# Kernel tuning notes

Hardware: AMD Instinct MI355X
Metric: run time of the kernel (lower is better)

The kernel has to match this reference:

```python
import jax, jax.numpy as jnp
import numpy as np

EPS = 1e-6

def _ln(x, g, b):
    m = jnp.mean(x, -1, keepdims=True)
    v = jnp.mean((x - m) ** 2, -1, keepdims=True)
    return (x - m) * jax.lax.rsqrt(v + 1e-5) * g + b

def _mha(qin, kin, vin, wq, bq, wk, bk, wv, bv, wo, bo, nh=8):
    B, T, D = qin.shape
    S = kin.shape[1]
    dh = D // nh
    q = (qin @ wq + bq).reshape(B, T, nh, dh)
    k = (kin @ wk + bk).reshape(B, S, nh, dh)
    v = (vin @ wv + bv).reshape(B, S, nh, dh)
    a = jax.nn.softmax(jnp.einsum('bthd,bshd->bhts', q, k) / np.float32(np.sqrt(dh)), -1)
    o = jnp.einsum('bhts,bshd->bthd', a, v).reshape(B, T, D)
    return o @ wo + bo

def _sinu_pe(pos, num_feats=128, temperature=20.0):
    # pos: [..., 2] (x, y); returns [..., 2*num_feats] ordered (y-feats, x-feats)
    dim_t = temperature ** ((2 * (jnp.arange(num_feats) // 2)) / num_feats)
    e = pos[..., None] * (2 * np.pi) / dim_t  # [..., 2, F]
    e = jnp.stack([jnp.sin(e[..., 0::2]), jnp.cos(e[..., 1::2])], -1).reshape(e.shape)
    return jnp.concatenate([e[..., 1, :], e[..., 0, :]], -1)

def _spatial36(b1, b2, sizes):
    # b1, b2: [B, Q, 4]; sizes: [B, 2] = (h, w). UPT-style 18 feats + log -> 36.
    h = sizes[:, 0:1]; w = sizes[:, 1:2]
    c1x = (b1[..., 0] + b1[..., 2]) / 2; c1y = (b1[..., 1] + b1[..., 3]) / 2
    c2x = (b2[..., 0] + b2[..., 2]) / 2; c2y = (b2[..., 1] + b2[..., 3]) / 2
    w1 = b1[..., 2] - b1[..., 0]; h1 = b1[..., 3] - b1[..., 1]
    w2 = b2[..., 2] - b2[..., 0]; h2 = b2[..., 3] - b2[..., 1]
    a1 = w1 * h1; a2 = w2 * h2
    dx = jnp.abs(c2x - c1x) / (w1 + EPS)
    dy = jnp.abs(c2y - c1y) / (h1 + EPS)
    ix = jnp.clip(jnp.minimum(b1[..., 2], b2[..., 2]) - jnp.maximum(b1[..., 0], b2[..., 0]), 0)
    iy = jnp.clip(jnp.minimum(b1[..., 3], b2[..., 3]) - jnp.maximum(b1[..., 1], b2[..., 1]), 0)
    inter = ix * iy
    iou = inter / (a1 + a2 - inter + EPS)
    f = jnp.stack([c1x / w, c1y / h, c2x / w, c2y / h, w1 / w, h1 / h, w2 / w, h2 / h,
                   a1 / (h * w), a2 / (h * w), a2 / (a1 + EPS), w1 / (h1 + EPS), w2 / (h2 + EPS), iou,
                   (c2x > c1x) * dx, (c2x < c1x) * dx, (c2y > c1y) * dy, (c2y < c1y) * dy], -1)
    return jnp.concatenate([f, jnp.log(f + EPS)], -1)

def _forward(boxes, embeds, image_sizes, pose, line, sw1, sb1, sw2, sb2, sw3, sb3, bw, bb, pw, pb, lw, lb, enc_pe_w, enc_pe_b, enc_qkv_w, enc_qkv_b, enc_out_w, enc_out_b, enc_ff1_w, enc_ff1_b, enc_ff2_w, enc_ff2_b, enc_ln1_g, enc_ln1_b, enc_ln2_g, enc_ln2_b, dec_q_w, dec_q_b, dec_kv_w, dec_kv_b, dec_out_w, dec_out_b, dec_ff1_w, dec_ff1_b, dec_ff2_w, dec_ff2_b, dec_ln1_g, dec_ln1_b, dec_ln2_g, dec_ln2_b, fc1_w, fc1_b, fc2_w, fc2_b, mln1_g, mln1_b, mln2_g, mln2_b, m1_w, m1_b, m2_w, m2_b, labels, nh):
    B, N, _ = boxes.shape
    # static human-object pairing (x != y) & (x < nh)
    xg, yg = np.meshgrid(np.arange(N), np.arange(N), indexing='ij')
    keep = (xg != yg) & (xg < nh)
    xk = jnp.asarray(xg[keep]); yk = jnp.asarray(yg[keep])  # [P]
    # line features: adaptive-avg-pool(1,1) + 1x1 conv == spatial mean + linear
    line_feat = jnp.mean(line, axis=(2, 3)) @ lw + lb  # [B, 256]
    # spatial head on all N*N ordered pairs, then gather kept pairs
    xa = jnp.asarray(xg.reshape(-1)); ya = jnp.asarray(yg.reshape(-1))
    f36 = _spatial36(boxes[:, xa], boxes[:, ya], image_sizes)  # [B, N*N, 36]
    s = jax.nn.relu(f36 @ sw1 + sb1)
    s = jax.nn.relu(s @ sw2 + sb2)
    s = jax.nn.relu(s @ sw3 + sb3)
    spa = s.reshape(B, N, N, -1)[:, xk, yk]  # [B, P, R]
    # box sinusoidal positional encodings (cat of centre-PE and wh-PE)
    whwh = image_sizes[:, jnp.array([1, 0, 1, 0])][:, None]  # [B,1,4]
    bxn = boxes / whwh
    ctr = (bxn[..., :2] + bxn[..., 2:]) / 2
    whb = bxn[..., 2:] - bxn[..., :2]
    box_pe = jnp.concatenate([_sinu_pe(ctr), _sinu_pe(whb)], -1)  # [B, N, 512]
    # 2-layer transformer encoder over instance tokens (pos added to q,k)
    posx = box_pe @ enc_pe_w + enc_pe_b
    x = embeds
    for i in range(enc_qkv_w.shape[0]):
        wq, wk_, wv = jnp.split(enc_qkv_w[i], 3, axis=1)
        bq, bk_, bv = jnp.split(enc_qkv_b[i], 3)
        qk = x + posx
        att = _mha(qk, qk, x, wq, bq, wk_, bk_, wv, bv, enc_out_w[i], enc_out_b[i])
        x = _ln(x + att, enc_ln1_g[i], enc_ln1_b[i])
        ff = jax.nn.relu(x @ enc_ff1_w[i] + enc_ff1_b[i]) @ enc_ff2_w[i] + enc_ff2_b[i]
        x = _ln(x + ff, enc_ln2_g[i], enc_ln2_b[i])
    # pair gather + human/object positional embeds (box PE projected + line feature)
    pe_h = box_pe[:, xk] @ bw + bb + line_feat[:, None, :]
    pe_o = box_pe[:, yk] @ bw + bb + line_feat[:, None, :]
    h = x[:, xk]; o = x[:, yk]  # [B, P, 256]
    pose_ctx = pose @ pw + pb  # [B, M, 256]
    # HO refine decoder: cross-attention from pair tokens to pose tokens
    for l in range(dec_q_w.shape[0]):
        wk_, wv = jnp.split(dec_kv_w[l], 2, axis=1)
        bk_, bv = jnp.split(dec_kv_b[l], 2)
        def _layer(feat, pe):
            att = _mha(feat + pe, pose_ctx, pose_ctx, dec_q_w[l], dec_q_b[l], wk_, bk_, wv, bv, dec_out_w[l], dec_out_b[l])
            feat = _ln(feat + att, dec_ln1_g[l], dec_ln1_b[l])
            ff = jax.nn.relu(feat @ dec_ff1_w[l] + dec_ff1_b[l]) @ dec_ff2_w[l] + dec_ff2_b[l]
            return _ln(feat + ff, dec_ln2_g[l], dec_ln2_b[l])
        h = _layer(h, pe_h)
        o = _layer(o, pe_o)
    # multi-modal fusion
    ho = jnp.concatenate([h, o], -1)  # [B, P, 512]
    ho = _ln(ho @ fc1_w + fc1_b, mln1_g, mln1_b)
    sp = _ln(spa @ fc2_w + fc2_b, mln2_g, mln2_b)
    z = jax.nn.relu(jnp.concatenate([ho, sp], -1))
    z = jax.nn.relu(z @ m1_w + m1_b)
    z = jax.nn.relu(z @ m2_w + m2_b)
    return z  # [B, P, 256] HOI query features

def setup_inputs() -> dict:
    key = jax.random.key(0)
    ks = iter(jax.random.split(key, 80))
    B, N, NH, M, HH, WW = 16, 128, 32, 64, 8, 8
    W = 0.05
    def rn(shape, s=1.0):
        return jax.random.normal(next(ks), shape, dtype=jnp.float32) * s
    def ru(shape):
        return jax.random.uniform(next(ks), shape, dtype=jnp.float32)
    sizes = 800.0 + 480.0 * ru((B, 2))  # (h, w)
    wh = sizes[:, jnp.array([1, 0])]
    xy = ru((B, N, 2)) * wh[:, None] * 0.7
    bwh = ru((B, N, 2)) * wh[:, None] * 0.25 + 4.0
    boxes = jnp.concatenate([xy, xy + bwh], -1)
    labels = jnp.concatenate([jnp.zeros((B, NH), jnp.int32), jax.random.randint(next(ks), (B, N - NH), 1, 81, dtype=jnp.int32)], -1)
    return dict(
        boxes=boxes, embeds=rn((B, N, 256)), image_sizes=sizes, pose=rn((B, M, 768)), line=rn((B, 2048, HH, WW)),
        sw1=rn((36, 128), W), sb1=jnp.zeros((128,)), sw2=rn((128, 256), W), sb2=jnp.zeros((256,)), sw3=rn((256, 256), W), sb3=jnp.zeros((256,)),
        bw=rn((512, 256), W), bb=jnp.zeros((256,)), pw=rn((768, 256), W), pb=jnp.zeros((256,)), lw=rn((2048, 256), W), lb=jnp.zeros((256,)),
        enc_pe_w=rn((512, 256), W), enc_pe_b=jnp.zeros((256,)),
        enc_qkv_w=rn((2, 256, 768), W), enc_qkv_b=jnp.zeros((2, 768)), enc_out_w=rn((2, 256, 256), W), enc_out_b=jnp.zeros((2, 256)),
        enc_ff1_w=rn((2, 256, 1024), W), enc_ff1_b=jnp.zeros((2, 1024)), enc_ff2_w=rn((2, 1024, 256), W), enc_ff2_b=jnp.zeros((2, 256)),
        enc_ln1_g=jnp.ones((2, 256)), enc_ln1_b=jnp.zeros((2, 256)), enc_ln2_g=jnp.ones((2, 256)), enc_ln2_b=jnp.zeros((2, 256)),
        dec_q_w=rn((2, 256, 256), W), dec_q_b=jnp.zeros((2, 256)), dec_kv_w=rn((2, 256, 512), W), dec_kv_b=jnp.zeros((2, 512)),
        dec_out_w=rn((2, 256, 256), W), dec_out_b=jnp.zeros((2, 256)),
        dec_ff1_w=rn((2, 256, 1024), W), dec_ff1_b=jnp.zeros((2, 1024)), dec_ff2_w=rn((2, 1024, 256), W), dec_ff2_b=jnp.zeros((2, 256)),
        dec_ln1_g=jnp.ones((2, 256)), dec_ln1_b=jnp.zeros((2, 256)), dec_ln2_g=jnp.ones((2, 256)), dec_ln2_b=jnp.zeros((2, 256)),
        fc1_w=rn((512, 256), W), fc1_b=jnp.zeros((256,)), fc2_w=rn((256, 256), W), fc2_b=jnp.zeros((256,)),
        mln1_g=jnp.ones((256,)), mln1_b=jnp.zeros((256,)), mln2_g=jnp.ones((256,)), mln2_b=jnp.zeros((256,)),
        m1_w=rn((512, 384), W), m1_b=jnp.zeros((384,)), m2_w=rn((384, 256), W), m2_b=jnp.zeros((256,)),
        labels=labels, nh=NH)

def reference(boxes, embeds, image_sizes, pose, line, sw1, sb1, sw2, sb2, sw3, sb3, bw, bb, pw, pb, lw, lb, enc_pe_w, enc_pe_b, enc_qkv_w, enc_qkv_b, enc_out_w, enc_out_b, enc_ff1_w, enc_ff1_b, enc_ff2_w, enc_ff2_b, enc_ln1_g, enc_ln1_b, enc_ln2_g, enc_ln2_b, dec_q_w, dec_q_b, dec_kv_w, dec_kv_b, dec_out_w, dec_out_b, dec_ff1_w, dec_ff1_b, dec_ff2_w, dec_ff2_b, dec_ln1_g, dec_ln1_b, dec_ln2_g, dec_ln2_b, fc1_w, fc1_b, fc2_w, fc2_b, mln1_g, mln1_b, mln2_g, mln2_b, m1_w, m1_b, m2_w, m2_b, labels, nh):
    return _forward(boxes, embeds, image_sizes, pose, line, sw1, sb1, sw2, sb2, sw3, sb3, bw, bb, pw, pb, lw, lb, enc_pe_w, enc_pe_b, enc_qkv_w, enc_qkv_b, enc_out_w, enc_out_b, enc_ff1_w, enc_ff1_b, enc_ff2_w, enc_ff2_b, enc_ln1_g, enc_ln1_b, enc_ln2_g, enc_ln2_b, dec_q_w, dec_q_b, dec_kv_w, dec_kv_b, dec_out_w, dec_out_b, dec_ff1_w, dec_ff1_b, dec_ff2_w, dec_ff2_b, dec_ln1_g, dec_ln1_b, dec_ln2_g, dec_ln2_b, fc1_w, fc1_b, fc2_w, fc2_b, mln1_g, mln1_b, mln2_g, mln2_b, m1_w, m1_b, m2_w, m2_b, labels, nh)
```

## Files before the change

kernel.cpp:

```cpp
#include <hip/hip_runtime.h>
#include <stdint.h>

static constexpr int B      = 16;
static constexpr int N      = 128;
static constexpr int P      = 4064;
static constexpr int MPOSE  = 64;
static constexpr int64_t BN = (int64_t)B * N;
static constexpr int64_t BP = (int64_t)B * P;

#define TWO_PI 6.283185307179586f
#define QSCALE 0.17677669529663687f

typedef __attribute__((ext_vector_type(4))) float f32x4;
typedef __attribute__((ext_vector_type(8))) short bf16x8;
typedef __attribute__((ext_vector_type(8))) unsigned short u16x8;
typedef __attribute__((ext_vector_type(4))) unsigned short u16x4;

__device__ __forceinline__ unsigned short f2bf(float f) {
    union { float f; unsigned u; } v; v.f = f;
    unsigned r = (v.u + 0x7fffu + ((v.u >> 16) & 1u)) >> 16;
    return (unsigned short)r;
}
__device__ __forceinline__ float bf2f(unsigned short u) {
    union { unsigned u; float f; } v; v.u = (unsigned)u << 16;
    return v.f;
}
__device__ __forceinline__ void pair_xy(int p, int& x, int& y) {
    x = p / 127;
    int r = p - x * 127;
    y = (r < x) ? r : r + 1;
}

struct WDesc { const float* src; int64_t dstOff; int K, Nn, Kpad, blockStart; };
struct WTable { WDesc d[29]; int nDesc; };

__global__ __launch_bounds__(256) void wprep_all_k(WTable t, unsigned short* __restrict__ wt)
{
    __shared__ float s[32][33];
    int bid = blockIdx.x;
    int di = 0;
    for (int i = 1; i < t.nDesc; ++i) if (t.d[i].blockStart <= bid) di = i;
    const WDesc& d = t.d[di];
    int lbid = bid - d.blockStart;
    int kTiles = d.Kpad >> 5;
    int k0 = (lbid % kTiles) * 32, n0 = (lbid / kTiles) * 32;
    int tx = threadIdx.x & 31, ty = threadIdx.x >> 5;
#pragma unroll
    for (int i = 0; i < 4; ++i) {
        int k = k0 + ty + i * 8;
        s[ty + i * 8][tx] = (k < d.K) ? d.src[(int64_t)k * d.Nn + n0 + tx] : 0.f;
    }
    __syncthreads();
    unsigned short* dst = wt + d.dstOff;
#pragma unroll
    for (int i = 0; i < 4; ++i) {
        int n = n0 + ty + i * 8;
        dst[(int64_t)n * d.Kpad + k0 + tx] = f2bf(s[tx][ty + i * 8]);
    }
}

template <bool RELU_OUT>
__global__ __launch_bounds__(256) void bgemm_k(
    const float* __restrict__ A, const float* __restrict__ A2, int lda,
    const unsigned short* __restrict__ Bt, int ldk,
    const float* __restrict__ bias,
    const float* __restrict__ Cadd, int addLd,
    const float* __restrict__ lfp,
    float* __restrict__ C, int ldc,
    int kSteps)
{
    __shared__ unsigned short As[128][40];
    __shared__ unsigned short Bs[128][40];
    const int tid  = threadIdx.x;
    const int lane = tid & 63;
    const int wave = tid >> 6;
    const int wr = wave >> 1, wc = wave & 1;
    const int row0 = blockIdx.y * 128, col0 = blockIdx.x * 128;
    const int l15 = lane & 15, l4 = lane >> 4;
    const int sr = tid >> 1;
    const int sh = (tid & 1) * 16;

    f32x4 acc[4][4] = {};

    for (int ks = 0; ks < kSteps; ++ks) {
        const int k0 = ks * 32;
        {
            const int64_t off = (int64_t)(row0 + sr) * lda + k0 + sh;
            const float* ap = A + off;
            float v[16];
#pragma unroll
            for (int i = 0; i < 4; ++i) {
                float4 tv = ((const float4*)ap)[i];
                v[i*4+0] = tv.x; v[i*4+1] = tv.y; v[i*4+2] = tv.z; v[i*4+3] = tv.w;
            }
            if (A2) {
                const float* ap2 = A2 + off;
#pragma unroll
                for (int i = 0; i < 4; ++i) {
                    float4 tv = ((const float4*)ap2)[i];
                    v[i*4+0] += tv.x; v[i*4+1] += tv.y; v[i*4+2] += tv.z; v[i*4+3] += tv.w;
                }
            }
            u16x8 p0, p1;
#pragma unroll
            for (int j = 0; j < 8; ++j) { p0[j] = f2bf(v[j]); p1[j] = f2bf(v[8 + j]); }
            *(u16x8*)&As[sr][sh]     = p0;
            *(u16x8*)&As[sr][sh + 8] = p1;
        }
        {
            const unsigned short* bp = Bt + (int64_t)(col0 + sr) * ldk + k0 + sh;
            *(u16x8*)&Bs[sr][sh]     = *(const u16x8*)bp;
            *(u16x8*)&Bs[sr][sh + 8] = *(const u16x8*)(bp + 8);
        }
        __syncthreads();
        bf16x8 af[4], bfr[4];
#pragma unroll
        for (int f = 0; f < 4; ++f) {
            af[f]  = *(const bf16x8*)&As[wr * 64 + f * 16 + l15][l4 * 8];
            bfr[f] = *(const bf16x8*)&Bs[wc * 64 + f * 16 + l15][l4 * 8];
        }
#pragma unroll
        for (int i = 0; i < 4; ++i)
#pragma unroll
            for (int j = 0; j < 4; ++j)
                acc[i][j] = __builtin_amdgcn_mfma_f32_16x16x32_bf16(af[i], bfr[j], acc[i][j], 0, 0, 0);
        __syncthreads();
    }
#pragma unroll
    for (int i = 0; i < 4; ++i) {
        int rb = row0 + wr * 64 + i * 16 + l4 * 4;
#pragma unroll
        for (int j = 0; j < 4; ++j) {
            int c = col0 + wc * 64 + j * 16 + l15;
            float bv = bias ? bias[c] : 0.f;
#pragma unroll
            for (int e = 0; e < 4; ++e) {
                int r = rb + e;
                float vv = acc[i][j][e] + bv;
                if (Cadd && c < addLd) vv += Cadd[(int64_t)r * addLd + c];
                if (lfp) vv += lfp[(r >> 7) * 256 + c];
                if (RELU_OUT) vv = fmaxf(vv, 0.f);
                C[(int64_t)r * ldc + c] = vv;
            }
        }
    }
}

static void bgemm(hipStream_t st,
                  const float* A, const float* A2, int lda,
                  const unsigned short* Bt, int ldk, const float* bias,
                  const float* Cadd, int addLd, const float* lfp,
                  float* C, int ldc, int M, int Ncols, int K, bool reluOut)
{
    dim3 g(Ncols / 128, M / 128), b(256);
    if (reluOut) bgemm_k<true><<<g,b,0,st>>>(A,A2,lda,Bt,ldk,bias,Cadd,addLd,lfp,C,ldc,K/32);
    else         bgemm_k<false><<<g,b,0,st>>>(A,A2,lda,Bt,ldk,bias,Cadd,addLd,lfp,C,ldc,K/32);
}

__global__ __launch_bounds__(256) void tgemm_k(
    const float* __restrict__ A, int lda,
    const unsigned short* __restrict__ Bt, int ldk,
    const float* __restrict__ bias,
    const float* __restrict__ res,
    const float* __restrict__ g, const float* __restrict__ be,
    float* __restrict__ C, int kSteps)
{
    __shared__ unsigned short As[64][40];
    __shared__ unsigned short Bs[256][40];
    __shared__ float partS[64][4], partQ[64][4];
    __shared__ float statM[64], statI[64];
    const int tid = threadIdx.x;
    const int lane = tid & 63, w = tid >> 6;
    const int l15 = lane & 15, l4 = lane >> 4;
    const int row0 = blockIdx.x * 64;
    const int sra = tid >> 2, sha = (tid & 3) * 8;

    f32x4 acc[4][4] = {};
    for (int ks = 0; ks < kSteps; ++ks) {
        int k0 = ks * 32;
        {
            const float* ap = A + (int64_t)(row0 + sra) * lda + k0 + sha;
            float4 t0 = ((const float4*)ap)[0];
            float4 t1 = ((const float4*)ap)[1];
            u16x8 p;
            p[0]=f2bf(t0.x); p[1]=f2bf(t0.y); p[2]=f2bf(t0.z); p[3]=f2bf(t0.w);
            p[4]=f2bf(t1.x); p[5]=f2bf(t1.y); p[6]=f2bf(t1.z); p[7]=f2bf(t1.w);
            *(u16x8*)&As[sra][sha] = p;
        }
        {
            const unsigned short* bp = Bt + (int64_t)tid * ldk + k0;
#pragma unroll
            for (int q = 0; q < 4; ++q)
                *(u16x8*)&Bs[tid][q * 8] = *(const u16x8*)(bp + q * 8);
        }
        __syncthreads();
        bf16x8 af[4], bfr[4];
#pragma unroll
        for (int f = 0; f < 4; ++f) {
            af[f]  = *(const bf16x8*)&As[f * 16 + l15][l4 * 8];
            bfr[f] = *(const bf16x8*)&Bs[w * 64 + f * 16 + l15][l4 * 8];
        }
#pragma unroll
        for (int i = 0; i < 4; ++i)
#pragma unroll
            for (int j = 0; j < 4; ++j)
                acc[i][j] = __builtin_amdgcn_mfma_f32_16x16x32_bf16(af[i], bfr[j], acc[i][j], 0, 0, 0);
        __syncthreads();
    }
    float ps[4][4] = {}, pq[4][4] = {};
#pragma unroll
    for (int i = 0; i < 4; ++i)
#pragma unroll
    for (int j = 0; j < 4; ++j) {
        int c = w * 64 + j * 16 + l15;
#pragma unroll
        for (int e = 0; e < 4; ++e) {
            int r = i * 16 + l4 * 4 + e;
            float v = acc[i][j][e] + bias[c] + res[(int64_t)(row0 + r) * 256 + c];
            acc[i][j][e] = v;
            ps[i][e] += v;
            pq[i][e] += v * v;
        }
    }
#pragma unroll
    for (int i = 0; i < 4; ++i)
#pragma unroll
    for (int e = 0; e < 4; ++e) {
#pragma unroll
        for (int m = 1; m < 16; m <<= 1) {
            ps[i][e] += __shfl_xor(ps[i][e], m);
            pq[i][e] += __shfl_xor(pq[i][e], m);
        }
    }
    if (l15 == 0) {
#pragma unroll
        for (int i = 0; i < 4; ++i)
#pragma unroll
        for (int e = 0; e < 4; ++e) {
            int r = i * 16 + l4 * 4 + e;
            partS[r][w] = ps[i][e];
            partQ[r][w] = pq[i][e];
        }
    }
    __syncthreads();
    if (tid < 64) {
        float s = partS[tid][0] + partS[tid][1] + partS[tid][2] + partS[tid][3];
        float q = partQ[tid][0] + partQ[tid][1] + partQ[tid][2] + partQ[tid][3];
        float m = s * (1.f/256.f);
        float var = q * (1.f/256.f) - m * m;
        statM[tid] = m;
        statI[tid] = rsqrtf(var + 1e-5f);
    }
    __syncthreads();
#pragma unroll
    for (int i = 0; i < 4; ++i)
#pragma unroll
    for (int j = 0; j < 4; ++j) {
        int c = w * 64 + j * 16 + l15;
#pragma unroll
        for (int e = 0; e < 4; ++e) {
            int r = i * 16 + l4 * 4 + e;
            C[(int64_t)(row0 + r) * 256 + c] = (acc[i][j][e] - statM[r]) * statI[r] * g[c] + be[c];
        }
    }
}

template <bool RELU_OUT, bool RELU_A, bool OUT_BF16>
__global__ __launch_bounds__(256) void hgemm_k(
    const unsigned short* __restrict__ A, int lda,
    const unsigned short* __restrict__ Bt, int ldk,
    const float* __restrict__ bias,
    void* __restrict__ Cv, int ldc,
    int kSteps)
{
    __shared__ unsigned short As[128][40];
    __shared__ unsigned short Bs[128][40];
    const int tid  = threadIdx.x;
    const int lane = tid & 63;
    const int wave = tid >> 6;
    const int wr = wave >> 1, wc = wave & 1;
    const int row0 = blockIdx.y * 128, col0 = blockIdx.x * 128;
    const int l15 = lane & 15, l4 = lane >> 4;
    const int sr = tid >> 1;
    const int sh = (tid & 1) * 16;

    f32x4 acc[4][4] = {};

    for (int ks = 0; ks < kSteps; ++ks) {
        const int k0 = ks * 32;
        {
            const unsigned short* ap = A + (int64_t)(row0 + sr) * lda + k0 + sh;
            u16x8 q0 = *(const u16x8*)ap;
            u16x8 q1 = *(const u16x8*)(ap + 8);
            if (RELU_A) {
#pragma unroll
                for (int q = 0; q < 8; ++q) {
                    q0[q] = (q0[q] & 0x8000u) ? 0 : q0[q];
                    q1[q] = (q1[q] & 0x8000u) ? 0 : q1[q];
                }
            }
            *(u16x8*)&As[sr][sh]     = q0;
            *(u16x8*)&As[sr][sh + 8] = q1;
        }
        {
            const unsigned short* bp = Bt + (int64_t)(col0 + sr) * ldk + k0 + sh;
            *(u16x8*)&Bs[sr][sh]     = *(const u16x8*)bp;
            *(u16x8*)&Bs[sr][sh + 8] = *(const u16x8*)(bp + 8);
        }
        __syncthreads();
        bf16x8 af[4], bfr[4];
#pragma unroll
        for (int f = 0; f < 4; ++f) {
            af[f]  = *(const bf16x8*)&As[wr * 64 + f * 16 + l15][l4 * 8];
            bfr[f] = *(const bf16x8*)&Bs[wc * 64 + f * 16 + l15][l4 * 8];
        }
#pragma unroll
        for (int i = 0; i < 4; ++i)
#pragma unroll
            for (int j = 0; j < 4; ++j)
                acc[i][j] = __builtin_amdgcn_mfma_f32_16x16x32_bf16(af[i], bfr[j], acc[i][j], 0, 0, 0);
        __syncthreads();
    }
#pragma unroll
    for (int i = 0; i < 4; ++i) {
        int rb = row0 + wr * 64 + i * 16 + l4 * 4;
#pragma unroll
        for (int j = 0; j < 4; ++j) {
            int c = col0 + wc * 64 + j * 16 + l15;
            float bv = bias ? bias[c] : 0.f;
#pragma unroll
            for (int e = 0; e < 4; ++e) {
                int64_t off = (int64_t)(rb + e) * ldc + c;
                float vv = acc[i][j][e] + bv;
                if (RELU_OUT) vv = fmaxf(vv, 0.f);
                if (OUT_BF16) ((unsigned short*)Cv)[off] = f2bf(vv);
                else          ((float*)Cv)[off] = vv;
            }
        }
    }
}

__global__ __launch_bounds__(256) void spa_k(
    const float* __restrict__ boxes, const float* __restrict__ sizes,
    const unsigned short* __restrict__ W1, const float* __restrict__ b1,
    const unsigned short* __restrict__ W2, const float* __restrict__ b2,
    unsigned short* __restrict__ t3out, int chunk0)
{
    __shared__ unsigned short F[128][72];
    __shared__ unsigned short Bs[128][40];
    __shared__ unsigned short D1s[128][136];
    const int tid  = threadIdx.x;
    const int lane = tid & 63;
    const int wave = tid >> 6;
    const int wr = wave >> 1, wc = wave & 1;
    const int row0 = blockIdx.x * 128;
    const int l15 = lane & 15, l4 = lane >> 4;
    const int sr = tid >> 1;
    const int sh = (tid & 1) * 16;

    if (tid < 128) {
        int gp = chunk0 + row0 + tid;
        int b = gp / P, p = gp - b * P;
        int xi, yi; pair_xy(p, xi, yi);
        const float* b1x = boxes + ((int64_t)b * N + xi) * 4;
        const float* b2x = boxes + ((int64_t)b * N + yi) * 4;
        float h = sizes[b * 2 + 0], w = sizes[b * 2 + 1];
        float c1x = (b1x[0] + b1x[2]) * 0.5f, c1y = (b1x[1] + b1x[3]) * 0.5f;
        float c2x = (b2x[0] + b2x[2]) * 0.5f, c2y = (b2x[1] + b2x[3]) * 0.5f;
        float w1 = b1x[2] - b1x[0], h1 = b1x[3] - b1x[1];
        float w2 = b2x[2] - b2x[0], h2 = b2x[3] - b2x[1];
        float a1 = w1 * h1, a2 = w2 * h2;
        float dx = fabsf(c2x - c1x) / (w1 + 1e-6f);
        float dy = fabsf(c2y - c1y) / (h1 + 1e-6f);
        float ix = fmaxf(fminf(b1x[2], b2x[2]) - fmaxf(b1x[0], b2x[0]), 0.f);
        float iy = fmaxf(fminf(b1x[3], b2x[3]) - fmaxf(b1x[1], b2x[1]), 0.f);
        float inter = ix * iy;
        float iou = inter / (a1 + a2 - inter + 1e-6f);
        float f[18];
        f[0] = c1x / w;  f[1] = c1y / h;  f[2] = c2x / w;  f[3] = c2y / h;
        f[4] = w1 / w;   f[5] = h1 / h;   f[6] = w2 / w;   f[7] = h2 / h;
        f[8] = a1 / (h * w); f[9] = a2 / (h * w); f[10] = a2 / (a1 + 1e-6f);
        f[11] = w1 / (h1 + 1e-6f); f[12] = w2 / (h2 + 1e-6f); f[13] = iou;
        f[14] = (c2x > c1x) ? dx : 0.f;  f[15] = (c2x < c1x) ? dx : 0.f;
        f[16] = (c2y > c1y) ? dy : 0.f;  f[17] = (c2y < c1y) ? dy : 0.f;
#pragma unroll
        for (int i = 0; i < 18; ++i) {
            F[tid][i]      = f2bf(f[i]);
            F[tid][18 + i] = f2bf(logf(f[i] + 1e-6f));
        }
#pragma unroll
        for (int i = 36; i < 64; ++i) F[tid][i] = 0;
    }
    __syncthreads();

    f32x4 acc1[4][4] = {};
    for (int ks = 0; ks < 2; ++ks) {
        const int k0 = ks * 32;
        {
            const unsigned short* bp = W1 + (int64_t)sr * 64 + k0 + sh;
            *(u16x8*)&Bs[sr][sh]     = *(const u16x8*)bp;
            *(u16x8*)&Bs[sr][sh + 8] = *(const u16x8*)(bp + 8);
        }
        __syncthreads();
        bf16x8 af[4], bfr[4];
#pragma unroll
        for (int f = 0; f < 4; ++f) {
            af[f]  = *(const bf16x8*)&F[wr * 64 + f * 16 + l15][k0 + l4 * 8];
            bfr[f] = *(const bf16x8*)&Bs[wc * 64 + f * 16 + l15][l4 * 8];
        }
#pragma unroll
        for (int i = 0; i < 4; ++i)
#pragma unroll
            for (int j = 0; j < 4; ++j)
                acc1[i][j] = __builtin_amdgcn_mfma_f32_16x16x32_bf16(af[i], bfr[j], acc1[i][j], 0, 0, 0);
        __syncthreads();
    }
#pragma unroll
    for (int i = 0; i < 4; ++i) {
        int rb = wr * 64 + i * 16 + l4 * 4;
#pragma unroll
        for (int j = 0; j < 4; ++j) {
            int c = wc * 64 + j * 16 + l15;
            float bv = b1[c];
#pragma unroll
            for (int e = 0; e < 4; ++e)
                D1s[rb + e][c] = f2bf(fmaxf(acc1[i][j][e] + bv, 0.f));
        }
    }
    __syncthreads();

    f32x4 acc2[2][4][4] = {};
#pragma unroll
    for (int n = 0; n < 2; ++n) {
        for (int kk = 0; kk < 4; ++kk) {
            {
                const unsigned short* bp = W2 + (int64_t)(n * 128 + sr) * 128 + kk * 32 + sh;
                *(u16x8*)&Bs[sr][sh]     = *(const u16x8*)bp;
                *(u16x8*)&Bs[sr][sh + 8] = *(const u16x8*)(bp + 8);
            }
            __syncthreads();
            bf16x8 af[4], bfr[4];
#pragma unroll
            for (int f = 0; f < 4; ++f) {
                af[f]  = *(const bf16x8*)&D1s[wr * 64 + f * 16 + l15][kk * 32 + l4 * 8];
                bfr[f] = *(const bf16x8*)&Bs[wc * 64 + f * 16 + l15][l4 * 8];
            }
#pragma unroll
            for (int i = 0; i < 4; ++i)
#pragma unroll
                for (int j = 0; j < 4; ++j)
                    acc2[n][i][j] = __builtin_amdgcn_mfma_f32_16x16x32_bf16(af[i], bfr[j], acc2[n][i][j], 0, 0, 0);
            __syncthreads();
        }
    }
#pragma unroll
    for (int n = 0; n < 2; ++n)
#pragma unroll
    for (int i = 0; i < 4; ++i) {
        int rb = row0 + wr * 64 + i * 16 + l4 * 4;
#pragma unroll
        for (int j = 0; j < 4; ++j) {
            int c = n * 128 + wc * 64 + j * 16 + l15;
            float bv = b2[c];
#pragma unroll
            for (int e = 0; e < 4; ++e)
                t3out[(int64_t)(rb + e) * 256 + c] = f2bf(fmaxf(acc2[n][i][j][e] + bv, 0.f));
        }
    }
}

__global__ __launch_bounds__(256) void sw3fc2ln_k(
    const unsigned short* __restrict__ A,
    const unsigned short* __restrict__ W1, const float* __restrict__ b1,
    const unsigned short* __restrict__ W2, const float* __restrict__ b2,
    const float* __restrict__ g, const float* __restrict__ be,
    unsigned short* __restrict__ outp, int ldo)
{
    __shared__ unsigned short As[128][40];
    __shared__ unsigned short Bs[128][40];
    __shared__ unsigned short D1s[128][136];
    __shared__ float partS[128][2], partQ[128][2];
    __shared__ float statM[128], statI[128];
    const int tid  = threadIdx.x;
    const int lane = tid & 63;
    const int wave = tid >> 6;
    const int wr = wave >> 1, wc = wave & 1;
    const int row0 = blockIdx.x * 128;
    const int l15 = lane & 15, l4 = lane >> 4;
    const int sr = tid >> 1;
    const int sh = (tid & 1) * 16;

    f32x4 acc2[2][4][4] = {};
    for (int j = 0; j < 2; ++j) {
        f32x4 acc1[4][4] = {};
        for (int ks = 0; ks < 8; ++ks) {
            const int k0 = ks * 32;
            {
                const unsigned short* ap = A + (int64_t)(row0 + sr) * 256 + k0 + sh;
                *(u16x8*)&As[sr][sh]     = *(const u16x8*)ap;
                *(u16x8*)&As[sr][sh + 8] = *(const u16x8*)(ap + 8);
            }
            {
                const unsigned short* bp = W1 + (int64_t)(j * 128 + sr) * 256 + k0 + sh;
                *(u16x8*)&Bs[sr][sh]     = *(const u16x8*)bp;
                *(u16x8*)&Bs[sr][sh + 8] = *(const u16x8*)(bp + 8);
            }
            __syncthreads();
            bf16x8 af[4], bfr[4];
#pragma unroll
            for (int f = 0; f < 4; ++f) {
                af[f]  = *(const bf16x8*)&As[wr * 64 + f * 16 + l15][l4 * 8];
                bfr[f] = *(const bf16x8*)&Bs[wc * 64 + f * 16 + l15][l4 * 8];
            }
#pragma unroll
            for (int i = 0; i < 4; ++i)
#pragma unroll
                for (int jj = 0; jj < 4; ++jj)
                    acc1[i][jj] = __builtin_amdgcn_mfma_f32_16x16x32_bf16(af[i], bfr[jj], acc1[i][jj], 0, 0, 0);
            __syncthreads();
        }
#pragma unroll
        for (int i = 0; i < 4; ++i) {
            int rb = wr * 64 + i * 16 + l4 * 4;
#pragma unroll
            for (int jj = 0; jj < 4; ++jj) {
                int c = wc * 64 + jj * 16 + l15;
                float bv = b1[j * 128 + c];
#pragma unroll
                for (int e = 0; e < 4; ++e)
                    D1s[rb + e][c] = f2bf(fmaxf(acc1[i][jj][e] + bv, 0.f));
            }
        }
        __syncthreads();
#pragma unroll
        for (int n = 0; n < 2; ++n) {
            for (int kk = 0; kk < 4; ++kk) {
                {
                    const unsigned short* bp = W2 + (int64_t)(n * 128 + sr) * 256 + j * 128 + kk * 32 + sh;
                    *(u16x8*)&Bs[sr][sh]     = *(const u16x8*)bp;
                    *(u16x8*)&Bs[sr][sh + 8] = *(const u16x8*)(bp + 8);
                }
                __syncthreads();
                bf16x8 af[4], bfr[4];
#pragma unroll
                for (int f = 0; f < 4; ++f) {
                    af[f]  = *(const bf16x8*)&D1s[wr * 64 + f * 16 + l15][kk * 32 + l4 * 8];
                    bfr[f] = *(const bf16x8*)&Bs[wc * 64 + f * 16 + l15][l4 * 8];
                }
#pragma unroll
                for (int i = 0; i < 4; ++i)
#pragma unroll
                    for (int jj = 0; jj < 4; ++jj)
                        acc2[n][i][jj] = __builtin_amdgcn_mfma_f32_16x16x32_bf16(af[i], bfr[jj], acc2[n][i][jj], 0, 0, 0);
                __syncthreads();
            }
        }
    }
    float ps[4][4] = {}, pq[4][4] = {};
#pragma unroll
    for (int n = 0; n < 2; ++n)
#pragma unroll
    for (int i = 0; i < 4; ++i)
#pragma unroll
    for (int jj = 0; jj < 4; ++jj) {
        int c = n * 128 + wc * 64 + jj * 16 + l15;
#pragma unroll
        for (int e = 0; e < 4; ++e) {
            float v = acc2[n][i][jj][e] + b2[c];
            acc2[n][i][jj][e] = v;
            ps[i][e] += v;
            pq[i][e] += v * v;
        }
    }
#pragma unroll
    for (int i = 0; i < 4; ++i)
#pragma unroll
    for (int e = 0; e < 4; ++e) {
#pragma unroll
        for (int m = 1; m < 16; m <<= 1) {
            ps[i][e] += __shfl_xor(ps[i][e], m);
            pq[i][e] += __shfl_xor(pq[i][e], m);
        }
    }
    if (l15 == 0) {
#pragma unroll
        for (int i = 0; i < 4; ++i)
#pragma unroll
        for (int e = 0; e < 4; ++e) {
            int r = wr * 64 + i * 16 + l4 * 4 + e;
            partS[r][wc] = ps[i][e];
            partQ[r][wc] = pq[i][e];
        }
    }
    __syncthreads();
    if (tid < 128) {
        float s = partS[tid][0] + partS[tid][1];
        float q = partQ[tid][0] + partQ[tid][1];
        float m = s * (1.f/256.f);
        float var = q * (1.f/256.f) - m * m;
        statM[tid] = m;
        statI[tid] = rsqrtf(var + 1e-5f);
    }
    __syncthreads();
#pragma unroll
    for (int n = 0; n < 2; ++n)
#pragma unroll
    for (int i = 0; i < 4; ++i)
#pragma unroll
    for (int jj = 0; jj < 4; ++jj) {
        int c = n * 128 + wc * 64 + jj * 16 + l15;
#pragma unroll
        for (int e = 0; e < 4; ++e) {
            int r = wr * 64 + i * 16 + l4 * 4 + e;
            float o = (acc2[n][i][jj][e] - statM[r]) * statI[r] * g[c] + be[c];
            outp[(int64_t)(row0 + r) * ldo + c] = f2bf(o);
        }
    }
}

__global__ __launch_bounds__(256) void pairln_k(
    const float* __restrict__ UV, const float* __restrict__ fb,
    const float* __restrict__ g, const float* __restrict__ be,
    unsigned short* __restrict__ outp, int ldo, int chunk0, int rows)
{
    int wave = threadIdx.x >> 6, lane = threadIdx.x & 63;
    int li = blockIdx.x * 4 + wave;
    if (li >= rows) return;
    int gp = chunk0 + li;
    int b = gp / P, p = gp - b * P;
    int xi, yi; pair_xy(p, xi, yi);
    int c = lane * 4;
    float4 u  = *(const float4*)(UV + ((int64_t)(b * 128 + xi)) * 512 + c);
    float4 vv = *(const float4*)(UV + ((int64_t)(b * 128 + yi)) * 512 + 256 + c);
    float4 fbv = *(const float4*)(fb + c);
    float4 v;
    v.x = u.x + vv.x + fbv.x; v.y = u.y + vv.y + fbv.y;
    v.z = u.z + vv.z + fbv.z; v.w = u.w + vv.w + fbv.w;
    float s  = v.x + v.y + v.z + v.w;
    float sq = v.x*v.x + v.y*v.y + v.z*v.z + v.w*v.w;
#pragma unroll
    for (int off = 1; off < 64; off <<= 1) {
        s  += __shfl_xor(s, off);
        sq += __shfl_xor(sq, off);
    }
    float m = s * (1.f/256.f);
    float var = sq * (1.f/256.f) - m * m;
    float inv = rsqrtf(var + 1e-5f);
    float4 gg = *(const float4*)(g + c);
    float4 bb = *(const float4*)(be + c);
    u16x4 o;
    o[0] = f2bf((v.x - m) * inv * gg.x + bb.x);
    o[1] = f2bf((v.y - m) * inv * gg.y + bb.y);
    o[2] = f2bf((v.z - m) * inv * gg.z + bb.z);
    o[3] = f2bf((v.w - m) * inv * gg.w + bb.w);
    *(u16x4*)(outp + (int64_t)li * ldo + c) = o;
}

__global__ __launch_bounds__(256) void line_mean_k(const float* __restrict__ line, float* __restrict__ lm)
{
    int wave = threadIdx.x >> 6, lane = threadIdx.x & 63;
    int bc = blockIdx.x * 4 + wave;
    float v = line[(int64_t)bc * 64 + lane];
#pragma unroll
    for (int off = 1; off < 64; off <<= 1) v += __shfl_xor(v, off);
    if (lane == 0) lm[bc] = v * (1.f/64.f);
}

__global__ __launch_bounds__(256) void line_proj_k(
    const float* __restrict__ lm, const float* __restrict__ lw,
    const float* __restrict__ lb, float* __restrict__ lf)
{
    __shared__ float red[8][32];
    int b = blockIdx.y, jg = blockIdx.x;
    int jj = threadIdx.x & 31, cc = threadIdx.x >> 5;
    int j = jg * 32 + jj;
    const float* lmb = lm + (int64_t)b * 2048 + cc * 256;
    const float* lwp = lw + (int64_t)(cc * 256) * 256 + j;
    float acc = 0.f;
#pragma unroll 4
    for (int k = 0; k < 256; ++k) acc += lmb[k] * lwp[(int64_t)k * 256];
    red[cc][jj] = acc;
    __syncthreads();
    if (cc == 0) {
        float s = lb[j];
#pragma unroll
        for (int i = 0; i < 8; ++i) s += red[i][jj];
        lf[b * 256 + j] = s;
    }
}

__global__ __launch_bounds__(512) void boxpe_k(
    const float* __restrict__ boxes, const float* __restrict__ sizes, float* __restrict__ boxpe)
{
    int row = blockIdx.x;
    int b = row >> 7;
    int i = threadIdx.x;
    const float* bx = boxes + (int64_t)row * 4;
    float h = sizes[b * 2 + 0], w = sizes[b * 2 + 1];
    float x0 = bx[0] / w, y0 = bx[1] / h, x1 = bx[2] / w, y1 = bx[3] / h;
    int seg = i >> 7, j = i & 127, k = j >> 1;
    float val;
    switch (seg) {
        case 0: val = (y0 + y1) * 0.5f; break;
        case 1: val = (x0 + x1) * 0.5f; break;
        case 2: val = (y1 - y0); break;
        default: val = (x1 - x0); break;
    }
    float dimt = exp2f((float)k * (4.321928094887362f / 64.f));
    float arg = val * TWO_PI / dimt;
    boxpe[(int64_t)row * 512 + i] = (j & 1) ? cosf(arg) : sinf(arg);
}

__global__ __launch_bounds__(128) void enc_attn_k(
    const float* __restrict__ qkv, float* __restrict__ outp)
{
    int b = blockIdx.x >> 3, hd = blockIdx.x & 7;
    __shared__ float kl[128][32];
    __shared__ float vl[128][32];
    int tid = threadIdx.x;
    for (int i = tid; i < 128 * 32; i += 128) {
        int s = i >> 5, j = i & 31;
        const float* rp = qkv + ((int64_t)(b * 128 + s)) * 768 + hd * 32 + j;
        kl[s][j] = rp[256];
        vl[s][j] = rp[512];
    }
    __syncthreads();
    int t = tid;
    const float* qp = qkv + ((int64_t)(b * 128 + t)) * 768 + hd * 32;
    float qr[32];
#pragma unroll
    for (int j = 0; j < 32; ++j) qr[j] = qp[j] * QSCALE;
    float m = -1e30f, l = 0.f;
    for (int s = 0; s < 128; ++s) {
        float d = 0.f;
#pragma unroll
        for (int j = 0; j < 32; ++j) d += qr[j] * kl[s][j];
        float mn = fmaxf(m, d);
        l = l * __expf(m - mn) + __expf(d - mn);
        m = mn;
    }
    float acc[32] = {};
    for (int s = 0; s < 128; ++s) {
        float d = 0.f;
#pragma unroll
        for (int j = 0; j < 32; ++j) d += qr[j] * kl[s][j];
        float wgt = __expf(d - m);
#pragma unroll
        for (int j = 0; j < 32; ++j) acc[j] += wgt * vl[s][j];
    }
    float linv = 1.f / l;
    float* op = outp + ((int64_t)(b * 128 + t)) * 256 + hd * 32;
#pragma unroll
    for (int j = 0; j < 32; ++j) op[j] = acc[j] * linv;
}

__global__ __launch_bounds__(256) void dec_attn_k(
    const float* __restrict__ q, const float* __restrict__ kv,
    float* __restrict__ outp, int rows, int rpb)
{
    int hd = blockIdx.y;
    int r0 = blockIdx.x * 256;
    __shared__ float kl[2][64][32];
    __shared__ float vl[2][64][32];
    int tid = threadIdx.x;
    int b0 = r0 / rpb;
    int b1 = (r0 + 255) / rpb;
    if (b1 >= B) b1 = B - 1;
    for (int i = tid; i < 64 * 32; i += 256) {
        int s = i >> 5, j = i & 31;
        int64_t off0 = ((int64_t)(b0 * MPOSE + s)) * 512 + hd * 32 + j;
        int64_t off1 = ((int64_t)(b1 * MPOSE + s)) * 512 + hd * 32 + j;
        kl[0][s][j] = kv[off0];
        vl[0][s][j] = kv[off0 + 256];
        kl[1][s][j] = kv[off1];
        vl[1][s][j] = kv[off1 + 256];
    }
    __syncthreads();
    int r = r0 + tid;
    if (r >= rows) return;
    int which = (r / rpb == b0) ? 0 : 1;
    int64_t qoff = (int64_t)r * 256 + hd * 32;
    float qr[32];
#pragma unroll
    for (int j = 0; j < 32; ++j) qr[j] = q[qoff + j] * QSCALE;
    float m = -1e30f, l = 0.f;
    for (int s = 0; s < 64; ++s) {
        float d = 0.f;
#pragma unroll
        for (int j = 0; j < 32; ++j) d += qr[j] * kl[which][s][j];
        float mn = fmaxf(m, d);
        l = l * __expf(m - mn) + __expf(d - mn);
        m = mn;
    }
    float acc[32] = {};
    for (int s = 0; s < 64; ++s) {
        float d = 0.f;
#pragma unroll
        for (int j = 0; j < 32; ++j) d += qr[j] * kl[which][s][j];
        float wgt = __expf(d - m);
#pragma unroll
        for (int j = 0; j < 32; ++j) acc[j] += wgt * vl[which][s][j];
    }
    float linv = 1.f / l;
#pragma unroll
    for (int j = 0; j < 32; ++j) outp[qoff + j] = acc[j] * linv;
}

static constexpr int64_t WT_QKV  = 0;
static constexpr int64_t WT_EOUT = WT_QKV  + 2*196608;
static constexpr int64_t WT_EFF1 = WT_EOUT + 2*65536;
static constexpr int64_t WT_EFF2 = WT_EFF1 + 2*262144;
static constexpr int64_t WT_DQ   = WT_EFF2 + 2*262144;
static constexpr int64_t WT_DKV  = WT_DQ   + 2*65536;
static constexpr int64_t WT_DOUT = WT_DKV  + 2*131072;
static constexpr int64_t WT_DFF1 = WT_DOUT + 2*65536;
static constexpr int64_t WT_DFF2 = WT_DFF1 + 2*262144;
static constexpr int64_t WT_SW1  = WT_DFF2 + 2*262144;
static constexpr int64_t WT_SW2  = WT_SW1 + 8192;
static constexpr int64_t WT_SW3  = WT_SW2 + 32768;
static constexpr int64_t WT_BW   = WT_SW3 + 65536;
static constexpr int64_t WT_PW   = WT_BW  + 131072;
static constexpr int64_t WT_EPE  = WT_PW  + 196608;
static constexpr int64_t WT_FC1  = WT_EPE + 131072;
static constexpr int64_t WT_FC2  = WT_FC1 + 131072;
static constexpr int64_t WT_M1   = WT_FC2 + 65536;
static constexpr int64_t WT_M2   = WT_M1  + 196608;
static constexpr int64_t WT_TOTAL = WT_M2 + 98304;

extern "C" void kernel_launch(void* const* d_in, const int* in_sizes, int n_in,
                              void* d_out, int out_size, void* d_ws, size_t ws_size,
                              hipStream_t stream)
{
    (void)in_sizes; (void)n_in; (void)out_size;
    const float* boxes     = (const float*)d_in[0];
    const float* embeds    = (const float*)d_in[1];
    const float* sizes     = (const float*)d_in[2];
    const float* pose      = (const float*)d_in[3];
    const float* line      = (const float*)d_in[4];
    const float* sw1 = (const float*)d_in[5];  const float* sb1 = (const float*)d_in[6];
    const float* sw2 = (const float*)d_in[7];  const float* sb2 = (const float*)d_in[8];
    const float* sw3 = (const float*)d_in[9];  const float* sb3 = (const float*)d_in[10];
    const float* bw  = (const float*)d_in[11]; const float* bb  = (const float*)d_in[12];
    const float* pw  = (const float*)d_in[13]; const float* pb  = (const float*)d_in[14];
    const float* lw  = (const float*)d_in[15]; const float* lb  = (const float*)d_in[16];
    const float* enc_pe_w  = (const float*)d_in[17]; const float* enc_pe_b = (const float*)d_in[18];
    const float* enc_qkv_w = (const float*)d_in[19]; const float* enc_qkv_b = (const float*)d_in[20];
    const float* enc_out_w = (const float*)d_in[21]; const float* enc_out_b = (const float*)d_in[22];
    const float* enc_ff1_w = (const float*)d_in[23]; const float* enc_ff1_b = (const float*)d_in[24];
    const float* enc_ff2_w = (const float*)d_in[25]; const float* enc_ff2_b = (const float*)d_in[26];
    const float* enc_ln1_g = (const float*)d_in[27]; const float* enc_ln1_b = (const float*)d_in[28];
    const float* enc_ln2_g = (const float*)d_in[29]; const float* enc_ln2_b = (const float*)d_in[30];
    const float* dec_q_w   = (const float*)d_in[31]; const float* dec_q_b  = (const float*)d_in[32];
    const float* dec_kv_w  = (const float*)d_in[33]; const float* dec_kv_b = (const float*)d_in[34];
    const float* dec_out_w = (const float*)d_in[35]; const float* dec_out_b = (const float*)d_in[36];
    const float* dec_ff1_w = (const float*)d_in[37]; const float* dec_ff1_b = (const float*)d_in[38];
    const float* dec_ff2_w = (const float*)d_in[39]; const float* dec_ff2_b = (const float*)d_in[40];
    const float* dec_ln1_g = (const float*)d_in[41]; const float* dec_ln1_b = (const float*)d_in[42];
    const float* dec_ln2_g = (const float*)d_in[43]; const float* dec_ln2_b = (const float*)d_in[44];
    const float* fc1_w = (const float*)d_in[45]; const float* fc1_b = (const float*)d_in[46];
    const float* fc2_w = (const float*)d_in[47]; const float* fc2_b = (const float*)d_in[48];
    const float* mln1_g = (const float*)d_in[49]; const float* mln1_b = (const float*)d_in[50];
    const float* mln2_g = (const float*)d_in[51]; const float* mln2_b = (const float*)d_in[52];
    const float* m1_w = (const float*)d_in[53]; const float* m1_b = (const float*)d_in[54];
    const float* m2_w = (const float*)d_in[55]; const float* m2_b = (const float*)d_in[56];
    float* out = (float*)d_out;

    float* base = (float*)d_ws;
    int64_t wsf = (int64_t)(ws_size / sizeof(float));
    float* x_   = base;
    float* bpw_ = x_   + 524288;
    float* lf   = bpw_ + 524288;
    float* kv0  = lf   + 4096;
    unsigned short* wt = (unsigned short*)(kv0 + 2 * 524288);
    float* arena = (float*)(wt + WT_TOTAL);
    const int64_t LIVE_F = arena - base;
    int64_t arena_f = wsf - LIVE_F;
    if (arena_f < 0) arena_f = 0;

    float* posx  = arena;
    float* boxpe = posx  + 524288;
    float* pqk0  = boxpe + 1048576;
    float* pqk1  = pqk0  + 1048576;
    float* e_qkv = pqk1  + 1048576;
    float* e_t   = e_qkv + 1572864;
    float* e_ff  = e_t   + 524288;
    float* pctx  = e_ff  + 2097152;
    float* lm    = pctx  + 262144;

    int64_t rc = ((arena_f * 2) / 1152) & ~127LL;
    if (rc > BP) rc = BP;
    if (rc < 128) rc = 128;

    {
        WTable T;
        int nd = 0, bs = 0;
        auto add = [&](const float* src, int64_t dstOff, int K, int Nn, int Kpad) {
            T.d[nd] = { src, dstOff, K, Nn, Kpad, bs };
            bs += (Kpad / 32) * (Nn / 32);
            ++nd;
        };
        for (int i = 0; i < 2; ++i) {
            add(enc_qkv_w + (int64_t)i*196608, WT_QKV  + i*196608, 256, 768, 256);
            add(enc_out_w + (int64_t)i*65536,  WT_EOUT + i*65536,  256, 256, 256);
            add(enc_ff1_w + (int64_t)i*262144, WT_EFF1 + i*262144, 256, 1024, 256);
            add(enc_ff2_w + (int64_t)i*262144, WT_EFF2 + i*262144, 1024, 256, 1024);
            add(dec_q_w   + (int64_t)i*65536,  WT_DQ   + i*65536,  256, 256, 256);
            add(dec_kv_w  + (int64_t)i*131072, WT_DKV  + i*131072, 256, 512, 256);
            add(dec_out_w + (int64_t)i*65536,  WT_DOUT + i*65536,  256, 256, 256);
            add(dec_ff1_w + (int64_t)i*262144, WT_DFF1 + i*262144, 256, 1024, 256);
            add(dec_ff2_w + (int64_t)i*262144, WT_DFF2 + i*262144, 1024, 256, 1024);
        }
        add(sw1, WT_SW1, 36, 128, 64);
        add(sw2, WT_SW2, 128, 256, 128);
        add(sw3, WT_SW3, 256, 256, 256);
        add(bw,  WT_BW,  512, 256, 512);
        add(pw,  WT_PW,  768, 256, 768);
        add(enc_pe_w, WT_EPE, 512, 256, 512);
        add(fc1_w,             WT_FC1,         256, 256, 256);
        add(fc1_w + 256 * 256, WT_FC1 + 65536, 256, 256, 256);
        add(fc2_w, WT_FC2, 256, 256, 256);
        add(m1_w, WT_M1, 512, 384, 512);
        add(m2_w, WT_M2, 384, 256, 384);
        T.nDesc = nd;
        wprep_all_k<<<bs, 256, 0, stream>>>(T, wt);
    }

    line_mean_k<<<8192, 256, 0, stream>>>(line, lm);
    line_proj_k<<<dim3(8, B), 256, 0, stream>>>(lm, lw, lb, lf);
    boxpe_k<<<(int)BN, 512, 0, stream>>>(boxes, sizes, boxpe);
    bgemm(stream, boxpe, nullptr, 512, wt + WT_EPE, 512, enc_pe_b, nullptr, 0, nullptr, posx, 256, (int)BN, 256, 512, false);
    bgemm(stream, boxpe, nullptr, 512, wt + WT_BW,  512, bb,       nullptr, 0, lf,      bpw_, 256, (int)BN, 256, 512, false);
    bgemm(stream, pose,  nullptr, 768, wt + WT_PW,  768, pb,       nullptr, 0, nullptr, pctx, 256, B*MPOSE, 256, 768, false);
    for (int l = 0; l < 2; ++l)
        bgemm(stream, pctx, nullptr, 256, wt + WT_DKV + l*131072, 256, dec_kv_b + (int64_t)l*512,
              nullptr, 0, nullptr, kv0 + (int64_t)l*524288, 512, B*MPOSE, 512, 256, false);
    bgemm(stream, posx, nullptr, 256, wt + WT_QKV,          256, nullptr, nullptr, 0, nullptr, pqk0, 512, (int)BN, 512, 256, false);
    bgemm(stream, posx, nullptr, 256, wt + WT_QKV + 196608, 256, nullptr, nullptr, 0, nullptr, pqk1, 512, (int)BN, 512, 256, false);

    for (int i = 0; i < 2; ++i) {
        const float* xin = (i == 0) ? embeds : x_;
        const float* pqk = (i == 0) ? pqk0 : pqk1;
        const unsigned short* Wq = wt + WT_QKV + (int64_t)i * 196608;
        bgemm(stream, xin, nullptr, 256, Wq, 256, enc_qkv_b + (int64_t)i*768, pqk, 512, nullptr,
              e_qkv, 768, (int)BN, 768, 256, false);
        enc_attn_k<<<B * 8, 128, 0, stream>>>(e_qkv, e_t);
        tgemm_k<<<(int)(BN / 64), 256, 0, stream>>>(e_t, 256, wt + WT_EOUT + (int64_t)i*65536, 256,
            enc_out_b + i*256, xin, enc_ln1_g + i*256, enc_ln1_b + i*256, x_, 8);
        bgemm(stream, x_, nullptr, 256, wt + WT_EFF1 + (int64_t)i*262144, 256, enc_ff1_b + i*1024,
              nullptr, 0, nullptr, e_ff, 1024, (int)BN, 1024, 256, true);
        tgemm_k<<<(int)(BN / 64), 256, 0, stream>>>(e_ff, 1024, wt + WT_EFF2 + (int64_t)i*262144, 1024,
            enc_ff2_b + i*256, x_, enc_ln2_g + i*256, enc_ln2_b + i*256, x_, 32);
    }

    for (int l = 0; l < 2; ++l) {
        bgemm(stream, x_, bpw_, 256, wt + WT_DQ + (int64_t)l*65536, 256, dec_q_b + l*256,
              nullptr, 0, nullptr, e_t, 256, (int)BN, 256, 256, false);
        dec_attn_k<<<dim3((int)(BN / 256), 8), 256, 0, stream>>>(e_t, kv0 + (int64_t)l*524288, e_qkv, (int)BN, N);
        tgemm_k<<<(int)(BN / 64), 256, 0, stream>>>(e_qkv, 256, wt + WT_DOUT + (int64_t)l*65536, 256,
            dec_out_b + l*256, x_, dec_ln1_g + l*256, dec_ln1_b + l*256, x_, 8);
        bgemm(stream, x_, nullptr, 256, wt + WT_DFF1 + (int64_t)l*262144, 256, dec_ff1_b + l*1024,
              nullptr, 0, nullptr, e_ff, 1024, (int)BN, 1024, 256, true);
        tgemm_k<<<(int)(BN / 64), 256, 0, stream>>>(e_ff, 1024, wt + WT_DFF2 + (int64_t)l*262144, 1024,
            dec_ff2_b + l*256, x_, dec_ln2_g + l*256, dec_ln2_b + l*256, x_, 32);
    }
    float* UV = kv0;
    bgemm(stream, x_, nullptr, 256, wt + WT_FC1, 256, nullptr, nullptr, 0, nullptr, UV, 512, (int)BN, 512, 256, false);

    for (int64_t c0 = 0; c0 < BP; c0 += rc) {
        int rows = (int)((BP - c0 < rc) ? (BP - c0) : rc);
        unsigned short* t3 = (unsigned short*)arena;
        unsigned short* zb = t3 + (int64_t)rc * 256;
        unsigned short* z2 = zb + (int64_t)rc * 512;

        spa_k<<<rows / 128, 256, 0, stream>>>(boxes, sizes,
            wt + WT_SW1, sb1, wt + WT_SW2, sb2, t3, (int)c0);
        sw3fc2ln_k<<<rows / 128, 256, 0, stream>>>(t3,
            wt + WT_SW3, sb3, wt + WT_FC2, fc2_b, mln2_g, mln2_b, zb + 256, 512);
        pairln_k<<<rows / 4, 256, 0, stream>>>(UV, fc1_b, mln1_g, mln1_b, zb, 512, (int)c0, rows);
        hgemm_k<true,true,true><<<dim3(3, rows / 128), 256, 0, stream>>>(
            zb, 512, wt + WT_M1, 512, m1_b, z2, 384, 16);
        hgemm_k<true,false,false><<<dim3(2, rows / 128), 256, 0, stream>>>(
            z2, 384, wt + WT_M2, 384, m2_b, out + c0 * 256, 256, 12);
    }
}
```

Measured before the change: 906.6 us.

## Split fused sw3+fc2+LayerNorm kernel into two generic GEMMs and a LayerNorm kernel

Replaces the single fused kernel that chained two 256x256 GEMMs with a LayerNorm epilogue by two launches of the existing hgemm_k plus a new one-wave-per-row LayerNorm kernel. The fused kernel ran one 128-row block per workgroup, had small tiles and many barriers, which limits parallelism. The split gives the GEMMs twice the grid and uses the tuned GEMM path. In exchange it adds intermediate bf16 round-trips through global memory, two extra launches, and an extra bf16 rounding before the LayerNorm.

```diff
diff --git a/kernel.cpp b/kernel.cpp
--- a/kernel.cpp
+++ b/kernel.cpp
@@ -469,153 +469,36 @@
     }
 }
 
-__global__ __launch_bounds__(256) void sw3fc2ln_k(
-    const unsigned short* __restrict__ A,
-    const unsigned short* __restrict__ W1, const float* __restrict__ b1,
-    const unsigned short* __restrict__ W2, const float* __restrict__ b2,
-    const float* __restrict__ g, const float* __restrict__ be,
-    unsigned short* __restrict__ outp, int ldo)
-{
-    __shared__ unsigned short As[128][40];
-    __shared__ unsigned short Bs[128][40];
-    __shared__ unsigned short D1s[128][136];
-    __shared__ float partS[128][2], partQ[128][2];
-    __shared__ float statM[128], statI[128];
-    const int tid  = threadIdx.x;
-    const int lane = tid & 63;
-    const int wave = tid >> 6;
-    const int wr = wave >> 1, wc = wave & 1;
-    const int row0 = blockIdx.x * 128;
-    const int l15 = lane & 15, l4 = lane >> 4;
-    const int sr = tid >> 1;
-    const int sh = (tid & 1) * 16;
-
-    f32x4 acc2[2][4][4] = {};
-    for (int j = 0; j < 2; ++j) {
-        f32x4 acc1[4][4] = {};
-        for (int ks = 0; ks < 8; ++ks) {
-            const int k0 = ks * 32;
-            {
-                const unsigned short* ap = A + (int64_t)(row0 + sr) * 256 + k0 + sh;
-                *(u16x8*)&As[sr][sh]     = *(const u16x8*)ap;
-                *(u16x8*)&As[sr][sh + 8] = *(const u16x8*)(ap + 8);
-            }
-            {
-                const unsigned short* bp = W1 + (int64_t)(j * 128 + sr) * 256 + k0 + sh;
-                *(u16x8*)&Bs[sr][sh]     = *(const u16x8*)bp;
-                *(u16x8*)&Bs[sr][sh + 8] = *(const u16x8*)(bp + 8);
-            }
-            __syncthreads();
-            bf16x8 af[4], bfr[4];
-#pragma unroll
-            for (int f = 0; f < 4; ++f) {
-                af[f]  = *(const bf16x8*)&As[wr * 64 + f * 16 + l15][l4 * 8];
-                bfr[f] = *(const bf16x8*)&Bs[wc * 64 + f * 16 + l15][l4 * 8];
-            }
-#pragma unroll
-            for (int i = 0; i < 4; ++i)
-#pragma unroll
-                for (int jj = 0; jj < 4; ++jj)
-                    acc1[i][jj] = __builtin_amdgcn_mfma_f32_16x16x32_bf16(af[i], bfr[jj], acc1[i][jj], 0, 0, 0);
-            __syncthreads();
-        }
-#pragma unroll
-        for (int i = 0; i < 4; ++i) {
-            int rb = wr * 64 + i * 16 + l4 * 4;
-#pragma unroll
-            for (int jj = 0; jj < 4; ++jj) {
-                int c = wc * 64 + jj * 16 + l15;
-                float bv = b1[j * 128 + c];
-#pragma unroll
-                for (int e = 0; e < 4; ++e)
-                    D1s[rb + e][c] = f2bf(fmaxf(acc1[i][jj][e] + bv, 0.f));
-            }
-        }
-        __syncthreads();
-#pragma unroll
-        for (int n = 0; n < 2; ++n) {
-            for (int kk = 0; kk < 4; ++kk) {
-                {
-                    const unsigned short* bp = W2 + (int64_t)(n * 128 + sr) * 256 + j * 128 + kk * 32 + sh;
-                    *(u16x8*)&Bs[sr][sh]     = *(const u16x8*)bp;
-                    *(u16x8*)&Bs[sr][sh + 8] = *(const u16x8*)(bp + 8);
-                }
-                __syncthreads();
-                bf16x8 af[4], bfr[4];
-#pragma unroll
-                for (int f = 0; f < 4; ++f) {
-                    af[f]  = *(const bf16x8*)&D1s[wr * 64 + f * 16 + l15][kk * 32 + l4 * 8];
-                    bfr[f] = *(const bf16x8*)&Bs[wc * 64 + f * 16 + l15][l4 * 8];
-                }
-#pragma unroll
-                for (int i = 0; i < 4; ++i)
-#pragma unroll
-                    for (int jj = 0; jj < 4; ++jj)
-                        acc2[n][i][jj] = __builtin_amdgcn_mfma_f32_16x16x32_bf16(af[i], bfr[jj], acc2[n][i][jj], 0, 0, 0);
-                __syncthreads();
-            }
-        }
-    }
-    float ps[4][4] = {}, pq[4][4] = {};
-#pragma unroll
-    for (int n = 0; n < 2; ++n)
-#pragma unroll
-    for (int i = 0; i < 4; ++i)
-#pragma unroll
-    for (int jj = 0; jj < 4; ++jj) {
-        int c = n * 128 + wc * 64 + jj * 16 + l15;
-#pragma unroll
-        for (int e = 0; e < 4; ++e) {
-            float v = acc2[n][i][jj][e] + b2[c];
-            acc2[n][i][jj][e] = v;
-            ps[i][e] += v;
-            pq[i][e] += v * v;
-        }
-    }
-#pragma unroll
-    for (int i = 0; i < 4; ++i)
-#pragma unroll
-    for (int e = 0; e < 4; ++e) {
-#pragma unroll
-        for (int m = 1; m < 16; m <<= 1) {
-            ps[i][e] += __shfl_xor(ps[i][e], m);
-            pq[i][e] += __shfl_xor(pq[i][e], m);
-        }
-    }
-    if (l15 == 0) {
-#pragma unroll
-        for (int i = 0; i < 4; ++i)
-#pragma unroll
-        for (int e = 0; e < 4; ++e) {
-            int r = wr * 64 + i * 16 + l4 * 4 + e;
-            partS[r][wc] = ps[i][e];
-            partQ[r][wc] = pq[i][e];
-        }
-    }
-    __syncthreads();
-    if (tid < 128) {
-        float s = partS[tid][0] + partS[tid][1];
-        float q = partQ[tid][0] + partQ[tid][1];
-        float m = s * (1.f/256.f);
-        float var = q * (1.f/256.f) - m * m;
-        statM[tid] = m;
-        statI[tid] = rsqrtf(var + 1e-5f);
-    }
-    __syncthreads();
-#pragma unroll
-    for (int n = 0; n < 2; ++n)
-#pragma unroll
-    for (int i = 0; i < 4; ++i)
-#pragma unroll
-    for (int jj = 0; jj < 4; ++jj) {
-        int c = n * 128 + wc * 64 + jj * 16 + l15;
-#pragma unroll
-        for (int e = 0; e < 4; ++e) {
-            int r = wr * 64 + i * 16 + l4 * 4 + e;
-            float o = (acc2[n][i][jj][e] - statM[r]) * statI[r] * g[c] + be[c];
-            outp[(int64_t)(row0 + r) * ldo + c] = f2bf(o);
-        }
-    }
+__global__ __launch_bounds__(256) void lnh_k(
+    unsigned short* __restrict__ outp, int ldo,
+    const unsigned short* __restrict__ x, int ldx,
+    const float* __restrict__ g, const float* __restrict__ be, int rows)
+{
+    int wave = threadIdx.x >> 6, lane = threadIdx.x & 63;
+    int row = blockIdx.x * 4 + wave;
+    if (row >= rows) return;
+    u16x4 u = *(const u16x4*)(x + (int64_t)row * ldx + lane * 4);
+    float4 v;
+    v.x = bf2f(u[0]); v.y = bf2f(u[1]); v.z = bf2f(u[2]); v.w = bf2f(u[3]);
+    float s  = v.x + v.y + v.z + v.w;
+    float sq = v.x*v.x + v.y*v.y + v.z*v.z + v.w*v.w;
+#pragma unroll
+    for (int off = 1; off < 64; off <<= 1) {
+        s  += __shfl_xor(s, off);
+        sq += __shfl_xor(sq, off);
+    }
+    float m = s * (1.f/256.f);
+    float var = sq * (1.f/256.f) - m * m;
+    float inv = rsqrtf(var + 1e-5f);
+    int c = lane * 4;
+    float4 gg = *(const float4*)(g + c);
+    float4 bb = *(const float4*)(be + c);
+    u16x4 o;
+    o[0] = f2bf((v.x - m) * inv * gg.x + bb.x);
+    o[1] = f2bf((v.y - m) * inv * gg.y + bb.y);
+    o[2] = f2bf((v.z - m) * inv * gg.z + bb.z);
+    o[3] = f2bf((v.w - m) * inv * gg.w + bb.w);
+    *(u16x4*)(outp + (int64_t)row * ldo + c) = o;
 }
 
 __global__ __launch_bounds__(256) void pairln_k(
@@ -974,8 +857,11 @@
 
         spa_k<<<rows / 128, 256, 0, stream>>>(boxes, sizes,
             wt + WT_SW1, sb1, wt + WT_SW2, sb2, t3, (int)c0);
-        sw3fc2ln_k<<<rows / 128, 256, 0, stream>>>(t3,
-            wt + WT_SW3, sb3, wt + WT_FC2, fc2_b, mln2_g, mln2_b, zb + 256, 512);
+        hgemm_k<true,false,true><<<dim3(2, rows / 128), 256, 0, stream>>>(
+            t3, 256, wt + WT_SW3, 256, sb3, z2, 256, 8);
+        hgemm_k<false,false,true><<<dim3(2, rows / 128), 256, 0, stream>>>(
+            z2, 256, wt + WT_FC2, 256, fc2_b, t3, 256, 8);
+        lnh_k<<<rows / 4, 256, 0, stream>>>(zb + 256, 512, t3, 256, mln2_g, mln2_b, rows);
         pairln_k<<<rows / 4, 256, 0, stream>>>(UV, fc1_b, mln1_g, mln1_b, zb, 512, (int)c0, rows);
         hgemm_k<true,true,true><<<dim3(3, rows / 128), 256, 0, stream>>>(
             zb, 512, wt + WT_M1, 512, m1_b, z2, 384, 16);
```

Measured after the change: 931.2 us. +2.7%, slower.
